# Kernel tuning notes

Hardware: AMD Instinct MI355X
Metric: run time of the kernel (lower is better)

Reference implementation:

```python
import jax, jax.numpy as jnp
import numpy as np

N_HEADS = 8
HEAD_DIM = 32
MODEL_DIM = N_HEADS * HEAD_DIM  # 256
IN_DIM = 256
N_MEM = 4
B, H, W = 4, 64, 64
SCALE = HEAD_DIM ** -0.5


def setup_inputs() -> dict:
    key = jax.random.key(0)
    ks = jax.random.split(key, 6)
    x = jax.random.normal(ks[0], (B, IN_DIM, H, W), dtype=jnp.float32)
    w_qkv = jax.random.normal(ks[1], (MODEL_DIM * 3, IN_DIM), dtype=jnp.float32) * 0.02
    b_qkv = jnp.zeros((MODEL_DIM * 3,), dtype=jnp.float32)
    mem_kv = jax.random.normal(ks[2], (2, N_HEADS, N_MEM, HEAD_DIM), dtype=jnp.float32)
    w_out = jax.random.normal(ks[3], (IN_DIM, MODEL_DIM), dtype=jnp.float32) * 0.02
    b_out = jnp.zeros((IN_DIM,), dtype=jnp.float32)
    return {"x": x, "w_qkv": w_qkv, "b_qkv": b_qkv, "mem_kv": mem_kv,
            "w_out": w_out, "b_out": b_out}


def reference(x, w_qkv, b_qkv, mem_kv, w_out, b_out):
    b, c, h, w = x.shape
    n = h * w
    # 1x1 conv == per-pixel matmul over channels
    qkv = jnp.einsum('bchw,oc->bohw', x, w_qkv) + b_qkv[None, :, None, None]
    q, k, v = jnp.split(qkv, 3, axis=1)
    # 'b (n d) h w -> b n (h w) d'
    def to_heads(t):
        return t.reshape(b, N_HEADS, HEAD_DIM, n).transpose(0, 1, 3, 2)
    q, k, v = to_heads(q), to_heads(k), to_heads(v)
    # prepend memory kv tokens: [b, n_heads, N_MEM + n, d]
    mk = jnp.broadcast_to(mem_kv[0][None], (b, N_HEADS, N_MEM, HEAD_DIM))
    mv = jnp.broadcast_to(mem_kv[1][None], (b, N_HEADS, N_MEM, HEAD_DIM))
    k = jnp.concatenate([mk, k], axis=-2)
    v = jnp.concatenate([mv, v], axis=-2)
    # scaled dot-product attention (dropout prob = 0 -> identity)
    sim = jnp.einsum('bnid,bnsd->bnis', q, k) * SCALE
    attn = jax.nn.softmax(sim, axis=-1)
    out = jnp.einsum('bnis,bnsd->bnid', attn, v)
    # 'b n (h w) d -> b (n d) h w'
    out = out.transpose(0, 1, 3, 2).reshape(b, MODEL_DIM, h, w)
    out = jnp.einsum('bchw,oc->bohw', out, w_out) + b_out[None, :, None, None]
    return out
```

## Files before the change

### kernel.cpp

```cpp
#include <hip/hip_runtime.h>
#include <stdint.h>


#define DEV static __device__ __forceinline__

typedef short s16x8 __attribute__((ext_vector_type(8)));
typedef float f32x4 __attribute__((ext_vector_type(4)));
typedef unsigned short u16x4 __attribute__((ext_vector_type(4)));
typedef unsigned short ushort_t;

DEV unsigned short f2b(float f) {
  unsigned u = __float_as_uint(f);
  u += 0x7fffu + ((u >> 16) & 1u);
  return (unsigned short)(u >> 16);
}

DEV void gld16(const void* g, void* l) {
  __builtin_amdgcn_global_load_lds(
      (const __attribute__((address_space(1))) unsigned int*)g,
      (__attribute__((address_space(3))) unsigned int*)l, 16, 0, 0);
}

__global__ __launch_bounds__(256) void pack_x(const float* __restrict__ x,
                                              ushort_t* __restrict__ xT) {
  __shared__ float t[64][65];
  const int b = blockIdx.z, cb = blockIdx.y, pb = blockIdx.x;
  const int tid = threadIdx.x;
#pragma unroll
  for (int i = 0; i < 16; ++i) {
    int idx = i * 256 + tid;
    int cl = idx >> 6, pl = idx & 63;
    t[cl][pl] = x[((size_t)(b * 256 + cb * 64 + cl)) * 4096 + pb * 64 + pl];
  }
  __syncthreads();
#pragma unroll
  for (int i = 0; i < 16; ++i) {
    int idx = i * 256 + tid;
    int pl = idx >> 6, cl = idx & 63;
    xT[((size_t)(b * 4096 + pb * 64 + pl)) * 256 + cb * 64 + cl] = f2b(t[cl][pl]);
  }
}

__global__ __launch_bounds__(256) void pack_small(
    const float* __restrict__ wqkv, const float* __restrict__ wout,
    const float* __restrict__ memkv, ushort_t* __restrict__ wqkvb,
    ushort_t* __restrict__ woutb, ushort_t* __restrict__ Kb,
    ushort_t* __restrict__ Vt) {
  int idx = blockIdx.x * 256 + threadIdx.x;
  if (idx < 196608) { wqkvb[idx] = f2b(wqkv[idx]); return; }
  idx -= 196608;
  if (idx < 65536) { woutb[idx] = f2b(wout[idx]); return; }
  idx -= 65536;
  if (idx < 131072) {
    int bh = idx >> 12, r = idx & 4095;
    int row = 4096 + (r >> 5), d = r & 31, h = bh & 7;
    float v = (row < 4100) ? memkv[h * 128 + (row - 4096) * 32 + d] : 0.f;
    Kb[((size_t)(bh * 4224 + row)) * 32 + d] = f2b(v);
    return;
  }
  idx -= 131072;
  {
    int bh = idx >> 12, r = idx & 4095;
    int d = r >> 7, col = 4096 + (r & 127), h = bh & 7;
    float v = (col < 4100) ? memkv[1024 + h * 128 + (col - 4096) * 32 + d] : 0.f;
    Vt[((size_t)(bh * 32 + d)) * 4224 + col] = f2b(v);
  }
}

__global__ __launch_bounds__(256) void qkv_gemm(
    const ushort_t* __restrict__ W, const ushort_t* __restrict__ X,
    const float* __restrict__ bias, ushort_t* __restrict__ Qb,
    ushort_t* __restrict__ Kb, ushort_t* __restrict__ Vt) {
  __shared__ ushort_t sA[128 * 32];
  __shared__ ushort_t sB[128 * 32];
  const int tid = threadIdx.x, wave = tid >> 6, lane = tid & 63;
  const int quad = lane >> 4, ln = lane & 15;
  const int b = blockIdx.z, my = blockIdx.y, nx = blockIdx.x;
  const int o0 = my * 128, p0 = nx * 128;
  const int wr = wave >> 1, wc = wave & 1;
  const ushort_t* Xb = X + (size_t)b * 4096 * 256;
  f32x4 acc[4][4];
#pragma unroll
  for (int i = 0; i < 4; ++i)
#pragma unroll
    for (int j = 0; j < 4; ++j) acc[i][j] = {0.f, 0.f, 0.f, 0.f};

  const int srow_in = lane >> 2, sgs = lane & 3;
  for (int kt = 0; kt < 8; ++kt) {
    const int k0 = kt * 32;
#pragma unroll
    for (int i2 = 0; i2 < 2; ++i2) {
      const int i = wave * 2 + i2;
      const int row = i * 16 + srow_in;
      const int gg = sgs ^ ((row >> 1) & 3);
      gld16(W + (size_t)(o0 + row) * 256 + k0 + gg * 8, sA + i * 512);
      gld16(Xb + (size_t)(p0 + row) * 256 + k0 + gg * 8, sB + i * 512);
    }
    __syncthreads();
    s16x8 af[4], bfv[4];
#pragma unroll
    for (int mt = 0; mt < 4; ++mt) {
      const int row = wr * 64 + mt * 16 + ln;
      af[mt] = *(const s16x8*)(sA + row * 32 + ((quad ^ ((row >> 1) & 3)) << 3));
    }
#pragma unroll
    for (int nt = 0; nt < 4; ++nt) {
      const int row = wc * 64 + nt * 16 + ln;
      bfv[nt] = *(const s16x8*)(sB + row * 32 + ((quad ^ ((row >> 1) & 3)) << 3));
    }
#pragma unroll
    for (int mt = 0; mt < 4; ++mt)
#pragma unroll
      for (int nt = 0; nt < 4; ++nt)
        acc[mt][nt] = __builtin_amdgcn_mfma_f32_16x16x32_bf16(af[mt], bfv[nt], acc[mt][nt], 0, 0, 0);
    __syncthreads();
  }
  const int region = o0 >> 8;
#pragma unroll
  for (int mt = 0; mt < 4; ++mt) {
#pragma unroll
    for (int r = 0; r < 4; ++r) {
      const int o_g = o0 + wr * 64 + mt * 16 + quad * 4 + r;
      const int rr = o_g & 255, h = rr >> 5, d = rr & 31;
      const int hb = b * 8 + h;
      const float bv = bias[o_g];
#pragma unroll
      for (int nt = 0; nt < 4; ++nt) {
        const int p_g = p0 + wc * 64 + nt * 16 + ln;
        const unsigned short w = f2b(acc[mt][nt][r] + bv);
        if (region == 0)      Qb[((size_t)(hb * 4096 + p_g)) * 32 + d] = w;
        else if (region == 1) Kb[((size_t)(hb * 4224 + p_g)) * 32 + d] = w;
        else                  Vt[((size_t)(hb * 32 + d)) * 4224 + p_g] = w;
      }
    }
  }
}

__global__ __launch_bounds__(256) void flash_attn(
    const ushort_t* __restrict__ Qb, const ushort_t* __restrict__ Kb,
    const ushort_t* __restrict__ Vt, ushort_t* __restrict__ AO) {
  __shared__ ushort_t sK[128 * 32];
  __shared__ ushort_t sV[32 * 128];
  __shared__ ushort_t sP[4 * 16 * 128];
  const int tid = threadIdx.x, wave = tid >> 6, lane = tid & 63;
  const int quad = lane >> 4, ln = lane & 15;
  const int bh = blockIdx.y, b = bh >> 3, h = bh & 7;
  const int q0 = blockIdx.x * 64 + wave * 16;
  const float CE = 0.17677669529663689f * 1.4426950408889634f;

  const s16x8 qf = *(const s16x8*)(Qb + ((size_t)(bh * 4096 + q0 + ln)) * 32 + quad * 8);
  f32x4 acc0 = {0.f, 0.f, 0.f, 0.f}, acc1 = {0.f, 0.f, 0.f, 0.f};
  float lsum = 0.f;
  ushort_t* myP = sP + wave * 2048;
  const int krow_in = lane >> 2, kgs = lane & 3;
  const int vrow_in = lane >> 4, vgs = lane & 15;

  for (int it = 0; it < 33; ++it) {
    const int kb = it << 7;
#pragma unroll
    for (int i2 = 0; i2 < 2; ++i2) {
      const int i = wave * 2 + i2;
      {
        const int row = i * 16 + krow_in;
        const int gg = kgs ^ ((row >> 1) & 3);
        gld16(Kb + ((size_t)(bh * 4224 + kb + row)) * 32 + gg * 8, sK + i * 512);
      }
      {
        const int d = i * 4 + vrow_in;
        const int gg = vgs ^ (d & 7);
        gld16(Vt + ((size_t)(bh * 32 + d)) * 4224 + kb + gg * 8, sV + i * 512);
      }
    }
    __syncthreads();
    float p[8][4];
#pragma unroll
    for (int t = 0; t < 8; ++t) {
      const int srow = t * 16 + ln;
      s16x8 kf = *(const s16x8*)(sK + srow * 32 + ((quad ^ ((srow >> 1) & 3)) << 3));
      f32x4 z = {0.f, 0.f, 0.f, 0.f};
      f32x4 s = __builtin_amdgcn_mfma_f32_16x16x32_bf16(kf, qf, z, 0, 0, 0);
#pragma unroll
      for (int r = 0; r < 4; ++r) p[t][r] = __builtin_amdgcn_exp2f(s[r] * CE);
    }
    if (it == 32) {
#pragma unroll
      for (int t = 0; t < 8; ++t)
#pragma unroll
        for (int r = 0; r < 4; ++r)
          p[t][r] = (t == 0 && quad == 0) ? p[t][r] : 0.f;
    }
#pragma unroll
    for (int t = 0; t < 8; ++t) lsum += (p[t][0] + p[t][1]) + (p[t][2] + p[t][3]);
#pragma unroll
    for (int t = 0; t < 8; ++t) {
#pragma unroll
      for (int r0 = 0; r0 < 4; r0 += 2) {
        const int k = t * 16 + quad * 4 + r0;
        const int adr = ln * 128 + (((k >> 3) ^ (ln & 7)) << 3) + (k & 7);
        unsigned pp = (unsigned)f2b(p[t][r0]) | ((unsigned)f2b(p[t][r0 + 1]) << 16);
        *(unsigned*)(myP + adr) = pp;
      }
    }
#pragma unroll
    for (int c = 0; c < 4; ++c) {
      s16x8 pf = *(const s16x8*)(myP + ln * 128 + ((((c << 2) + quad) ^ (ln & 7)) << 3));
#pragma unroll
      for (int hh = 0; hh < 2; ++hh) {
        const int d = hh * 16 + ln;
        s16x8 vf = *(const s16x8*)(sV + d * 128 + ((((c << 2) + quad) ^ (d & 7)) << 3));
        if (hh == 0) acc0 = __builtin_amdgcn_mfma_f32_16x16x32_bf16(vf, pf, acc0, 0, 0, 0);
        else         acc1 = __builtin_amdgcn_mfma_f32_16x16x32_bf16(vf, pf, acc1, 0, 0, 0);
      }
    }
    __syncthreads();
  }
  lsum += __shfl_xor(lsum, 16, 64);
  lsum += __shfl_xor(lsum, 32, 64);
  const float inv = 1.0f / lsum;
  ushort_t* dst = AO + ((size_t)(b * 4096 + q0 + ln)) * 256 + h * 32 + quad * 4;
  u16x4 o0v, o1v;
#pragma unroll
  for (int r = 0; r < 4; ++r) {
    o0v[r] = f2b(acc0[r] * inv);
    o1v[r] = f2b(acc1[r] * inv);
  }
  *(u16x4*)(dst) = o0v;
  *(u16x4*)(dst + 16) = o1v;
}

__global__ __launch_bounds__(256) void out_gemm(
    const ushort_t* __restrict__ W, const ushort_t* __restrict__ A,
    const float* __restrict__ bias, float* __restrict__ Out) {
  __shared__ ushort_t sA[128 * 32];
  __shared__ ushort_t sB[128 * 32];
  const int tid = threadIdx.x, wave = tid >> 6, lane = tid & 63;
  const int quad = lane >> 4, ln = lane & 15;
  const int b = blockIdx.z, my = blockIdx.y, nx = blockIdx.x;
  const int o0 = my * 128, p0 = nx * 128;
  const int wr = wave >> 1, wc = wave & 1;
  const ushort_t* Ab = A + (size_t)b * 4096 * 256;
  f32x4 acc[4][4];
#pragma unroll
  for (int i = 0; i < 4; ++i)
#pragma unroll
    for (int j = 0; j < 4; ++j) acc[i][j] = {0.f, 0.f, 0.f, 0.f};

  const int srow_in = lane >> 2, sgs = lane & 3;
  for (int kt = 0; kt < 8; ++kt) {
    const int k0 = kt * 32;
#pragma unroll
    for (int i2 = 0; i2 < 2; ++i2) {
      const int i = wave * 2 + i2;
      const int row = i * 16 + srow_in;
      const int gg = sgs ^ ((row >> 1) & 3);
      gld16(W + (size_t)(o0 + row) * 256 + k0 + gg * 8, sA + i * 512);
      gld16(Ab + (size_t)(p0 + row) * 256 + k0 + gg * 8, sB + i * 512);
    }
    __syncthreads();
    s16x8 af[4], bfv[4];
#pragma unroll
    for (int mt = 0; mt < 4; ++mt) {
      const int row = wr * 64 + mt * 16 + ln;
      af[mt] = *(const s16x8*)(sA + row * 32 + ((quad ^ ((row >> 1) & 3)) << 3));
    }
#pragma unroll
    for (int nt = 0; nt < 4; ++nt) {
      const int row = wc * 64 + nt * 16 + ln;
      bfv[nt] = *(const s16x8*)(sB + row * 32 + ((quad ^ ((row >> 1) & 3)) << 3));
    }
#pragma unroll
    for (int mt = 0; mt < 4; ++mt)
#pragma unroll
      for (int nt = 0; nt < 4; ++nt)
        acc[mt][nt] = __builtin_amdgcn_mfma_f32_16x16x32_bf16(af[mt], bfv[nt], acc[mt][nt], 0, 0, 0);
    __syncthreads();
  }
#pragma unroll
  for (int mt = 0; mt < 4; ++mt) {
#pragma unroll
    for (int r = 0; r < 4; ++r) {
      const int o_g = o0 + wr * 64 + mt * 16 + quad * 4 + r;
      const float bv = bias[o_g];
#pragma unroll
      for (int nt = 0; nt < 4; ++nt) {
        const int p_g = p0 + wc * 64 + nt * 16 + ln;
        Out[((size_t)(b * 256 + o_g)) * 4096 + p_g] = acc[mt][nt][r] + bv;
      }
    }
  }
}

extern "C" void kernel_launch(void* const* d_in, const int* in_sizes, int n_in,
                              void* d_out, int out_size, void* d_ws, size_t ws_size,
                              hipStream_t stream) {
  (void)in_sizes; (void)n_in; (void)out_size; (void)ws_size;
  const float* x      = (const float*)d_in[0];
  const float* w_qkv  = (const float*)d_in[1];
  const float* b_qkv  = (const float*)d_in[2];
  const float* mem_kv = (const float*)d_in[3];
  const float* w_out  = (const float*)d_in[4];
  const float* b_out  = (const float*)d_in[5];
  char* ws = (char*)d_ws;
  ushort_t* xT     = (ushort_t*)(ws);
  ushort_t* wqkvb  = (ushort_t*)(ws + 8388608);
  ushort_t* woutb  = (ushort_t*)(ws + 8781824);
  ushort_t* Qb     = (ushort_t*)(ws + 8912896);
  ushort_t* Kb     = (ushort_t*)(ws + 17301504);
  ushort_t* Vt     = (ushort_t*)(ws + 25952256);
  ushort_t* AO     = (ushort_t*)(ws + 34603008);
  float* out = (float*)d_out;

  pack_x<<<dim3(64, 4, 4), 256, 0, stream>>>(x, xT);
  pack_small<<<dim3(2048), 256, 0, stream>>>(w_qkv, w_out, mem_kv, wqkvb, woutb, Kb, Vt);
  qkv_gemm<<<dim3(32, 6, 4), 256, 0, stream>>>(wqkvb, xT, b_qkv, Qb, Kb, Vt);
  flash_attn<<<dim3(64, 32), 256, 0, stream>>>(Qb, Kb, Vt, AO);
  out_gemm<<<dim3(32, 2, 4), 256, 0, stream>>>(woutb, AO, b_out, out);
}
```

Baseline: 284.8 us.

## Cut attention LDS and conversion cost, fold softmax scale into Q, vectorize stores

The softmax scale times log2(e) is now folded into Q when the QKV GEMM writes it out, which removes a multiply per score in attention. The P staging buffer reuses sK after a barrier instead of using its own LDS region, and launch bounds request 8 blocks per CU to raise occupancy. A cheaper round-half-up bf16 conversion with perm-based packing replaces round-to-nearest-even, and the pack_x, QKV epilogue and attention output stores are widened. Costs are an extra barrier per iteration and slightly different bf16 rounding.

```diff
diff --git a/kernel.cpp b/kernel.cpp
--- a/kernel.cpp
+++ b/kernel.cpp
@@ -6,13 +6,14 @@
 
 typedef short s16x8 __attribute__((ext_vector_type(8)));
 typedef float f32x4 __attribute__((ext_vector_type(4)));
-typedef unsigned short u16x4 __attribute__((ext_vector_type(4)));
 typedef unsigned short ushort_t;
 
 DEV unsigned short f2b(float f) {
-  unsigned u = __float_as_uint(f);
-  u += 0x7fffu + ((u >> 16) & 1u);
-  return (unsigned short)(u >> 16);
+  return (unsigned short)((__float_as_uint(f) + 0x8000u) >> 16);
+}
+DEV unsigned pkf2b(float a, float b) {
+  return __builtin_amdgcn_perm(__float_as_uint(b) + 0x8000u,
+                               __float_as_uint(a) + 0x8000u, 0x07060302u);
 }
 
 DEV void gld16(const void* g, void* l) {
@@ -34,10 +35,11 @@
   }
   __syncthreads();
 #pragma unroll
-  for (int i = 0; i < 16; ++i) {
+  for (int i = 0; i < 8; ++i) {
     int idx = i * 256 + tid;
-    int pl = idx >> 6, cl = idx & 63;
-    xT[((size_t)(b * 4096 + pb * 64 + pl)) * 256 + cb * 64 + cl] = f2b(t[cl][pl]);
+    int pl = idx >> 5, c2 = idx & 31;
+    unsigned w = pkf2b(t[c2 * 2][pl], t[c2 * 2 + 1][pl]);
+    *(unsigned*)(xT + ((size_t)(b * 4096 + pb * 64 + pl)) * 256 + cb * 64 + c2 * 2) = w;
   }
 }
 
@@ -116,42 +118,51 @@
     __syncthreads();
   }
   const int region = o0 >> 8;
+  const float qs = (region == 0) ? (0.17677669529663689f * 1.4426950408889634f) : 1.0f;
 #pragma unroll
   for (int mt = 0; mt < 4; ++mt) {
-#pragma unroll
-    for (int r = 0; r < 4; ++r) {
-      const int o_g = o0 + wr * 64 + mt * 16 + quad * 4 + r;
-      const int rr = o_g & 255, h = rr >> 5, d = rr & 31;
-      const int hb = b * 8 + h;
-      const float bv = bias[o_g];
-#pragma unroll
-      for (int nt = 0; nt < 4; ++nt) {
-        const int p_g = p0 + wc * 64 + nt * 16 + ln;
-        const unsigned short w = f2b(acc[mt][nt][r] + bv);
-        if (region == 0)      Qb[((size_t)(hb * 4096 + p_g)) * 32 + d] = w;
-        else if (region == 1) Kb[((size_t)(hb * 4224 + p_g)) * 32 + d] = w;
-        else                  Vt[((size_t)(hb * 32 + d)) * 4224 + p_g] = w;
-      }
-    }
-  }
-}
-
-__global__ __launch_bounds__(256) void flash_attn(
+    const int obase = o0 + wr * 64 + mt * 16 + quad * 4;
+    const int rr = obase & 255;
+    const int h = rr >> 5, d0 = rr & 31;
+    const int hb = b * 8 + h;
+    const float4 bv = *(const float4*)(bias + obase);
+#pragma unroll
+    for (int nt = 0; nt < 4; ++nt) {
+      const int p_g = p0 + wc * 64 + nt * 16 + ln;
+      const float v0 = (acc[mt][nt][0] + bv.x) * qs;
+      const float v1 = (acc[mt][nt][1] + bv.y) * qs;
+      const float v2 = (acc[mt][nt][2] + bv.z) * qs;
+      const float v3 = (acc[mt][nt][3] + bv.w) * qs;
+      if (region == 0) {
+        *(uint2*)(Qb + ((size_t)(hb * 4096 + p_g)) * 32 + d0) =
+            make_uint2(pkf2b(v0, v1), pkf2b(v2, v3));
+      } else if (region == 1) {
+        *(uint2*)(Kb + ((size_t)(hb * 4224 + p_g)) * 32 + d0) =
+            make_uint2(pkf2b(v0, v1), pkf2b(v2, v3));
+      } else {
+        Vt[((size_t)(hb * 32 + d0 + 0)) * 4224 + p_g] = f2b(v0);
+        Vt[((size_t)(hb * 32 + d0 + 1)) * 4224 + p_g] = f2b(v1);
+        Vt[((size_t)(hb * 32 + d0 + 2)) * 4224 + p_g] = f2b(v2);
+        Vt[((size_t)(hb * 32 + d0 + 3)) * 4224 + p_g] = f2b(v3);
+      }
+    }
+  }
+}
+
+__global__ __launch_bounds__(256, 8) void flash_attn(
     const ushort_t* __restrict__ Qb, const ushort_t* __restrict__ Kb,
     const ushort_t* __restrict__ Vt, ushort_t* __restrict__ AO) {
   __shared__ ushort_t sK[128 * 32];
   __shared__ ushort_t sV[32 * 128];
-  __shared__ ushort_t sP[4 * 16 * 128];
   const int tid = threadIdx.x, wave = tid >> 6, lane = tid & 63;
   const int quad = lane >> 4, ln = lane & 15;
   const int bh = blockIdx.y, b = bh >> 3, h = bh & 7;
   const int q0 = blockIdx.x * 64 + wave * 16;
-  const float CE = 0.17677669529663689f * 1.4426950408889634f;
 
   const s16x8 qf = *(const s16x8*)(Qb + ((size_t)(bh * 4096 + q0 + ln)) * 32 + quad * 8);
   f32x4 acc0 = {0.f, 0.f, 0.f, 0.f}, acc1 = {0.f, 0.f, 0.f, 0.f};
-  float lsum = 0.f;
-  ushort_t* myP = sP + wave * 2048;
+  f32x4 ls4 = {0.f, 0.f, 0.f, 0.f};
+  ushort_t* myP = sK + wave * 1024;
   const int krow_in = lane >> 2, kgs = lane & 3;
   const int vrow_in = lane >> 4, vgs = lane & 15;
 
@@ -172,60 +183,56 @@
       }
     }
     __syncthreads();
-    float p[8][4];
+    unsigned pk[8][2];
 #pragma unroll
     for (int t = 0; t < 8; ++t) {
       const int srow = t * 16 + ln;
       s16x8 kf = *(const s16x8*)(sK + srow * 32 + ((quad ^ ((srow >> 1) & 3)) << 3));
       f32x4 z = {0.f, 0.f, 0.f, 0.f};
       f32x4 s = __builtin_amdgcn_mfma_f32_16x16x32_bf16(kf, qf, z, 0, 0, 0);
-#pragma unroll
-      for (int r = 0; r < 4; ++r) p[t][r] = __builtin_amdgcn_exp2f(s[r] * CE);
-    }
-    if (it == 32) {
-#pragma unroll
-      for (int t = 0; t < 8; ++t)
-#pragma unroll
-        for (int r = 0; r < 4; ++r)
-          p[t][r] = (t == 0 && quad == 0) ? p[t][r] : 0.f;
-    }
-#pragma unroll
-    for (int t = 0; t < 8; ++t) lsum += (p[t][0] + p[t][1]) + (p[t][2] + p[t][3]);
-#pragma unroll
-    for (int t = 0; t < 8; ++t) {
-#pragma unroll
-      for (int r0 = 0; r0 < 4; r0 += 2) {
-        const int k = t * 16 + quad * 4 + r0;
-        const int adr = ln * 128 + (((k >> 3) ^ (ln & 7)) << 3) + (k & 7);
-        unsigned pp = (unsigned)f2b(p[t][r0]) | ((unsigned)f2b(p[t][r0 + 1]) << 16);
-        *(unsigned*)(myP + adr) = pp;
-      }
-    }
-#pragma unroll
-    for (int c = 0; c < 4; ++c) {
-      s16x8 pf = *(const s16x8*)(myP + ln * 128 + ((((c << 2) + quad) ^ (ln & 7)) << 3));
-#pragma unroll
-      for (int hh = 0; hh < 2; ++hh) {
-        const int d = hh * 16 + ln;
-        s16x8 vf = *(const s16x8*)(sV + d * 128 + ((((c << 2) + quad) ^ (d & 7)) << 3));
-        if (hh == 0) acc0 = __builtin_amdgcn_mfma_f32_16x16x32_bf16(vf, pf, acc0, 0, 0, 0);
-        else         acc1 = __builtin_amdgcn_mfma_f32_16x16x32_bf16(vf, pf, acc1, 0, 0, 0);
-      }
-    }
-    __syncthreads();
-  }
+      f32x4 p;
+#pragma unroll
+      for (int r = 0; r < 4; ++r) p[r] = __builtin_amdgcn_exp2f(s[r]);
+      if (it == 32) {
+        if (!(t == 0 && quad == 0)) { p[0] = 0.f; p[1] = 0.f; p[2] = 0.f; p[3] = 0.f; }
+      }
+      ls4 += p;
+      pk[t][0] = pkf2b(p[0], p[1]);
+      pk[t][1] = pkf2b(p[2], p[3]);
+    }
+    __syncthreads();
+#pragma unroll
+    for (int h2 = 0; h2 < 2; ++h2) {
+#pragma unroll
+      for (int tt = 0; tt < 4; ++tt) {
+        const int t = h2 * 4 + tt;
+        const int off = ln * 64 + (((2 * tt + (quad >> 1)) ^ (ln & 7)) << 3) + ((quad & 1) << 2);
+        *(uint2*)(myP + off) = make_uint2(pk[t][0], pk[t][1]);
+      }
+#pragma unroll
+      for (int c = 0; c < 2; ++c) {
+        const int cg = h2 * 2 + c;
+        s16x8 pf = *(const s16x8*)(myP + ln * 64 + (((4 * c + quad) ^ (ln & 7)) << 3));
+#pragma unroll
+        for (int hh = 0; hh < 2; ++hh) {
+          const int d = hh * 16 + ln;
+          s16x8 vf = *(const s16x8*)(sV + d * 128 + (((cg * 4 + quad) ^ (d & 7)) << 3));
+          if (hh == 0) acc0 = __builtin_amdgcn_mfma_f32_16x16x32_bf16(vf, pf, acc0, 0, 0, 0);
+          else         acc1 = __builtin_amdgcn_mfma_f32_16x16x32_bf16(vf, pf, acc1, 0, 0, 0);
+        }
+      }
+    }
+    __syncthreads();
+  }
+  float lsum = (ls4[0] + ls4[1]) + (ls4[2] + ls4[3]);
   lsum += __shfl_xor(lsum, 16, 64);
   lsum += __shfl_xor(lsum, 32, 64);
   const float inv = 1.0f / lsum;
   ushort_t* dst = AO + ((size_t)(b * 4096 + q0 + ln)) * 256 + h * 32 + quad * 4;
-  u16x4 o0v, o1v;
-#pragma unroll
-  for (int r = 0; r < 4; ++r) {
-    o0v[r] = f2b(acc0[r] * inv);
-    o1v[r] = f2b(acc1[r] * inv);
-  }
-  *(u16x4*)(dst) = o0v;
-  *(u16x4*)(dst + 16) = o1v;
+  *(uint2*)(dst) = make_uint2(pkf2b(acc0[0] * inv, acc0[1] * inv),
+                              pkf2b(acc0[2] * inv, acc0[3] * inv));
+  *(uint2*)(dst + 16) = make_uint2(pkf2b(acc1[0] * inv, acc1[1] * inv),
+                                   pkf2b(acc1[2] * inv, acc1[3] * inv));
 }
 
 __global__ __launch_bounds__(256) void out_gemm(
```

Measured after the change: 241.7 us. -15.1%, faster.
